# Performance work log

Measured on AMD Instinct MI355X. Metric: run time of the kernel, lower is better.

## Reference

```python
import jax, jax.numpy as jnp
import numpy as np

VOCAB, E, H, L, N = 32000, 256, 512, 512, 64


def setup_inputs() -> dict:
    key = jax.random.key(0)
    ks = jax.random.split(key, 8)
    s_in = 1.0 / np.sqrt(H + E)
    return {
        "x": jax.random.randint(ks[0], (L, N), 0, VOCAB),
        "emb": jax.random.normal(ks[1], (VOCAB, E), dtype=jnp.float32),
        # weights stored (in, out); math identical to torch Linear with W.T
        "Wz": jax.random.uniform(ks[2], (H + E, H), jnp.float32, -s_in, s_in),
        "bz": jax.random.uniform(ks[3], (H,), jnp.float32, -s_in, s_in),
        "Wr": jax.random.uniform(ks[4], (H + E, H), jnp.float32, -s_in, s_in),
        "br": jax.random.uniform(ks[5], (H,), jnp.float32, -s_in, s_in),
        "Wh": jax.random.uniform(ks[6], (H + E, H), jnp.float32, -s_in, s_in),
        "bh": jax.random.uniform(ks[7], (H,), jnp.float32, -s_in, s_in),
    }


def reference(x, emb, Wz, bz, Wr, br, Wh, bh):
    # x: (L, N) int indices -> embedded once: (L, N, E)
    xe = emb[x]
    h0 = jnp.zeros((x.shape[1], Wz.shape[1]), dtype=emb.dtype)

    def step(h, e_t):
        hx = jnp.concatenate([h, e_t], axis=1)            # (N, H+E)
        z = jax.nn.sigmoid(hx @ Wz + bz)                  # update gate
        r = jax.nn.sigmoid(hx @ Wr + br)                  # reset gate
        rhx = jnp.concatenate([r * h, e_t], axis=1)
        h_tilde = jnp.tanh(rhx @ Wh + bh)
        h_new = (1.0 - z) * h + z * h_tilde
        return h_new, h_new

    _, hs = jax.lax.scan(step, h0, xe)                    # hs: (L, N, H)
    return hs
```

## Files before the change

### kernel.cpp

```cpp
#include <hip/hip_runtime.h>


#define LSTEPS 512
#define NBATCH 64
#define HDIM   512
#define EDIM   256
#define KDIM   768
#define NBLK   32
#define TPB    256

typedef _Float16 f16x8 __attribute__((ext_vector_type(8)));
typedef float    f32x4 __attribute__((ext_vector_type(4)));
typedef unsigned long long u64;

#define MFMA __builtin_amdgcn_mfma_f32_16x16x32_f16

__device__ __forceinline__ float sigm(float x){ return 1.0f/(1.0f+__expf(-x)); }
__device__ __forceinline__ float tanh_fast(float x){
  float e = __expf(2.0f*x);
  return 1.0f - 2.0f/(e + 1.0f);
}
__device__ __forceinline__ unsigned f16b(float x){
  union { _Float16 h; unsigned short u; } c; c.h = (_Float16)x; return (unsigned)c.u;
}

__global__ void prep_w(const float* __restrict__ Wz, const float* __restrict__ Wr,
                       const float* __restrict__ Wh, _Float16* __restrict__ wbuf){
  int tid = blockIdx.x*256 + threadIdx.x;
  int g   = tid / (HDIM*KDIM);
  int rem = tid - g*(HDIM*KDIM);
  int j   = rem / KDIM;
  int k   = rem - j*KDIM;
  const float* W = (g==0) ? Wz : ((g==1) ? Wr : Wh);
  wbuf[tid] = (_Float16)W[(size_t)k*HDIM + j];
}

__global__ void prep_emb(const int* __restrict__ x, const float* __restrict__ emb,
                         _Float16* __restrict__ ebuf){
  int tid = blockIdx.x*256 + threadIdx.x;
  int k4  = tid & 63;
  int tn  = tid >> 6;
  int row = x[tn];
  const float4 v = *(const float4*)(emb + (size_t)row*EDIM + (k4<<2));
  union { _Float16 h[4]; uint2 u; } p;
  p.h[0] = (_Float16)v.x; p.h[1] = (_Float16)v.y;
  p.h[2] = (_Float16)v.z; p.h[3] = (_Float16)v.w;
  *(uint2*)(ebuf + (size_t)tn*EDIM + (k4<<2)) = p.u;
}

__device__ __forceinline__ void store_x(_Float16* buf, int jc2, int n0, int lane,
                                        float v0, float v1, float v2, float v3){
  unsigned p01 = f16b(v0) | (f16b(v1) << 16);
  unsigned p23 = f16b(v2) | (f16b(v3) << 16);
  unsigned q01 = __shfl_xor(p01, 1, 64);
  unsigned q23 = __shfl_xor(p23, 1, 64);
  unsigned w0, w1; int r0;
  if (lane & 1){
    w0 = (q23 & 0xffffu) | (p23 << 16);
    w1 = (q23 >> 16)     | (p23 & 0xffff0000u);
    r0 = n0 + 2;
  } else {
    w0 = (p01 & 0xffffu) | (q01 << 16);
    w1 = (p01 >> 16)     | (q01 & 0xffff0000u);
    r0 = n0;
  }
  __hip_atomic_store((unsigned*)(buf + (size_t)r0*HDIM + jc2),     w0,
                     __ATOMIC_RELAXED, __HIP_MEMORY_SCOPE_AGENT);
  __hip_atomic_store((unsigned*)(buf + (size_t)(r0+1)*HDIM + jc2), w1,
                     __ATOMIC_RELAXED, __HIP_MEMORY_SCOPE_AGENT);
}

__device__ __forceinline__ void waitcnt_ge(const unsigned* c, unsigned target){
  for (;;){
    unsigned v = __hip_atomic_load(c, __ATOMIC_RELAXED, __HIP_MEMORY_SCOPE_AGENT);
    if (v >= target) break;
  }
}

__global__ __launch_bounds__(TPB, 1) void gru_persist(
    const _Float16* __restrict__ wbuf,
    const _Float16* __restrict__ ebuf,
    const float* __restrict__ bz, const float* __restrict__ br, const float* __restrict__ bh,
    _Float16* __restrict__ hx,
    _Float16* __restrict__ rhx,
    unsigned* __restrict__ cnth,
    unsigned* __restrict__ cntrh,
    float* __restrict__ out)
{
  __shared__ char wlds[3*16*1536];
  const int jbase = blockIdx.x * 16;

  for (int cidx = threadIdx.x; cidx < 3*16*96; cidx += TPB){
    int g   = cidx / (16*96);
    int rem = cidx - g*(16*96);
    int col = rem / 96;
    int kch = rem - col*96;
    const uint4 v = *(const uint4*)(wbuf + ((size_t)(g*HDIM + jbase + col))*KDIM + kch*8);
    int off = (((g*16 + col)*1536) + kch*16) ^ ((col & 7) << 4);
    *(uint4*)(wlds + off) = v;
  }
  __syncthreads();

  const int lane = threadIdx.x & 63;
  const int wave = threadIdx.x >> 6;
  const int c15  = lane & 15;
  const int kgrp = lane >> 4;
  const int jcol = jbase + c15;
  const int jc2  = jcol & ~1;
  const int arow = wave*16 + c15;
  const int n0   = wave*16 + kgrp*4;
  const int swz  = (c15 & 7) << 4;
  const int linz = ((      c15)*1536) + kgrp*16;
  const int linr = ((16  + c15)*1536) + kgrp*16;
  const int linh = ((32  + c15)*1536) + kgrp*16;
  const float bzj = bz[jcol];
  const float brj = br[jcol];
  const float bhj = bh[jcol];
  unsigned* mycnth  = cnth  + wave*32;
  unsigned* mycntrh = cntrh + wave*32;
  const u64* hrow  = (const u64*)hx  + (size_t)arow*128 + kgrp*2;
  const u64* rhrow = (const u64*)rhx + (size_t)arow*128 + kgrp*2;
  float hreg[4] = {0.f, 0.f, 0.f, 0.f};

  u64 q[32];
  f16x8 aereg[8];

#define LOADX(BASE) do {                                                      \
    _Pragma("unroll")                                                         \
    for (int kc = 0; kc < 16; ++kc){                                          \
      q[2*kc]   = __hip_atomic_load((BASE) + kc*8,     __ATOMIC_RELAXED,      \
                                    __HIP_MEMORY_SCOPE_AGENT);                \
      q[2*kc+1] = __hip_atomic_load((BASE) + kc*8 + 1, __ATOMIC_RELAXED,      \
                                    __HIP_MEMORY_SCOPE_AGENT);                \
    }                                                                         \
  } while (0)

#define AFRAG(KC) ({ union { u64 d[2]; f16x8 v; } _a;                         \
                     _a.d[0] = q[2*(KC)]; _a.d[1] = q[2*(KC)+1]; _a.v; })

  {
    const _Float16* ae0 = ebuf + (size_t)arow*EDIM + kgrp*8;
    #pragma unroll
    for (int kc = 0; kc < 8; ++kc) aereg[kc] = *(const f16x8*)(ae0 + kc*32);
  }

  for (int t = 0; t < LSTEPS; ++t){
    const unsigned tgt_h  = 32u*(unsigned)t;
    const unsigned tgt_rh = 32u*(unsigned)(t + 1);

    f32x4 accr = {0.f,0.f,0.f,0.f};
    #pragma unroll
    for (int kc = 0; kc < 8; ++kc){
      f16x8 brv = *(const f16x8*)(wlds + ((linr + (16+kc)*64) ^ swz));
      accr = MFMA(aereg[kc], brv, accr, 0, 0, 0);
    }
    waitcnt_ge(mycnth, tgt_h);
    LOADX(hrow);
    #pragma unroll
    for (int kc = 0; kc < 16; ++kc){
      f16x8 brv = *(const f16x8*)(wlds + ((linr + kc*64) ^ swz));
      accr = MFMA(AFRAG(kc), brv, accr, 0, 0, 0);
    }
    float rh[4];
    #pragma unroll
    for (int i = 0; i < 4; ++i)
      rh[i] = sigm(accr[i] + brj) * hreg[i];
    store_x(rhx, jc2, n0, lane, rh[0], rh[1], rh[2], rh[3]);
    asm volatile("s_waitcnt vmcnt(0)" ::: "memory");
    __builtin_amdgcn_sched_barrier(0);
    if (lane == 0)
      __hip_atomic_fetch_add(mycntrh, 1u,
                             __ATOMIC_RELAXED, __HIP_MEMORY_SCOPE_AGENT);

    f32x4 accz = {0.f,0.f,0.f,0.f};
    f32x4 acch = {0.f,0.f,0.f,0.f};
    #pragma unroll
    for (int kc = 0; kc < 16; ++kc){
      f16x8 bzv = *(const f16x8*)(wlds + ((linz + kc*64) ^ swz));
      accz = MFMA(AFRAG(kc), bzv, accz, 0, 0, 0);
    }
    #pragma unroll
    for (int kc = 0; kc < 8; ++kc){
      f16x8 bzv = *(const f16x8*)(wlds + ((linz + (16+kc)*64) ^ swz));
      f16x8 bhv = *(const f16x8*)(wlds + ((linh + (16+kc)*64) ^ swz));
      accz = MFMA(aereg[kc], bzv, accz, 0, 0, 0);
      acch = MFMA(aereg[kc], bhv, acch, 0, 0, 0);
    }
    float zreg[4];
    #pragma unroll
    for (int i = 0; i < 4; ++i) zreg[i] = sigm(accz[i] + bzj);

    waitcnt_ge(mycntrh, tgt_rh);
    LOADX(rhrow);
    #pragma unroll
    for (int kc = 0; kc < 16; ++kc){
      f16x8 bhv = *(const f16x8*)(wlds + ((linh + kc*64) ^ swz));
      acch = MFMA(AFRAG(kc), bhv, acch, 0, 0, 0);
    }
    #pragma unroll
    for (int i = 0; i < 4; ++i){
      float ht = tanh_fast(acch[i] + bhj);
      hreg[i] = hreg[i] + zreg[i]*(ht - hreg[i]);
    }
    store_x(hx, jc2, n0, lane, hreg[0], hreg[1], hreg[2], hreg[3]);
    asm volatile("s_waitcnt vmcnt(0)" ::: "memory");
    __builtin_amdgcn_sched_barrier(0);
    if (lane == 0)
      __hip_atomic_fetch_add(mycnth, 1u,
                             __ATOMIC_RELAXED, __HIP_MEMORY_SCOPE_AGENT);

    if (t + 1 < LSTEPS){
      const _Float16* aen = ebuf + ((size_t)(t+1)*NBATCH + arow)*EDIM + kgrp*8;
      #pragma unroll
      for (int kc = 0; kc < 8; ++kc) aereg[kc] = *(const f16x8*)(aen + kc*32);
    }
    #pragma unroll
    for (int i = 0; i < 4; ++i)
      out[((size_t)t*NBATCH + (n0+i))*HDIM + jcol] = hreg[i];
  }
#undef LOADX
#undef AFRAG
}

extern "C" void kernel_launch(void* const* d_in, const int* in_sizes, int n_in,
                              void* d_out, int out_size, void* d_ws, size_t ws_size,
                              hipStream_t stream) {
  const int*   x   = (const int*)  d_in[0];
  const float* emb = (const float*)d_in[1];
  const float* Wz  = (const float*)d_in[2];
  const float* bz  = (const float*)d_in[3];
  const float* Wr  = (const float*)d_in[4];
  const float* br  = (const float*)d_in[5];
  const float* Wh  = (const float*)d_in[6];
  const float* bh  = (const float*)d_in[7];
  float* out = (float*)d_out;
  char*  ws  = (char*)d_ws;

  size_t off = 0;
  unsigned* cnth  = (unsigned*)(ws + off); off += 4*32*4;
  unsigned* cntrh = (unsigned*)(ws + off); off += 4*32*4;
  _Float16* hx    = (_Float16*)(ws + off); off += (size_t)NBATCH*HDIM*2;
  size_t zero_bytes = off;
  _Float16* rhx   = (_Float16*)(ws + off); off += (size_t)NBATCH*HDIM*2;
  _Float16* wbuf  = (_Float16*)(ws + off); off += (size_t)3*HDIM*KDIM*2;
  _Float16* ebuf  = (_Float16*)(ws + off); off += (size_t)LSTEPS*NBATCH*EDIM*2;

  hipMemsetAsync(ws, 0, zero_bytes, stream);

  prep_w  <<<(3*HDIM*KDIM)/256,          256, 0, stream>>>(Wz, Wr, Wh, wbuf);
  prep_emb<<<(LSTEPS*NBATCH*EDIM/4)/256, 256, 0, stream>>>(x, emb, ebuf);
  gru_persist<<<NBLK, TPB, 0, stream>>>(wbuf, ebuf, bz, br, bh,
                                        hx, rhx, cnth, cntrh, out);
}
```

Measured before the change: 6.253 ms.

## Replace atomic step counters with per-block flags polled across lanes

Instead of every block doing a fetch_add on a shared per-wave counter, each block now stores the step index into its own flag slot. Waiters load all 32 block flags in parallel across lanes and leave the spin loop when every flag has reached the target. The out stores and the next-step embedding prefetch are moved off the critical path between releases, and the release now waits with a partial vmcnt so outstanding prefetch loads do not hold it up. The change also adds a startup probe that tests cross-XCD coherence of a flag/data pair and runs a burn loop if that test fails; this adds risk and possible overhead.

Result: no change. 6.302 ms (+0.8%).

```diff
diff --git a/kernel.cpp b/kernel.cpp
--- a/kernel.cpp
+++ b/kernel.cpp
@@ -70,10 +70,11 @@
                      __ATOMIC_RELAXED, __HIP_MEMORY_SCOPE_AGENT);
 }
 
-__device__ __forceinline__ void waitcnt_ge(const unsigned* c, unsigned target){
+__device__ __forceinline__ void waitfl(const unsigned* fl, unsigned target){
+  const int l31 = threadIdx.x & 31;
   for (;;){
-    unsigned v = __hip_atomic_load(c, __ATOMIC_RELAXED, __HIP_MEMORY_SCOPE_AGENT);
-    if (v >= target) break;
+    unsigned v = __hip_atomic_load(&fl[l31], __ATOMIC_RELAXED, __HIP_MEMORY_SCOPE_AGENT);
+    if (__all(v >= target)) break;
   }
 }
 
@@ -83,11 +84,15 @@
     const float* __restrict__ bz, const float* __restrict__ br, const float* __restrict__ bh,
     _Float16* __restrict__ hx,
     _Float16* __restrict__ rhx,
-    unsigned* __restrict__ cnth,
-    unsigned* __restrict__ cntrh,
+    unsigned* __restrict__ hfl,
+    unsigned* __restrict__ rhfl,
+    unsigned* __restrict__ xcnt,
+    unsigned* __restrict__ cflag,
+    unsigned* __restrict__ cdata,
     float* __restrict__ out)
 {
   __shared__ char wlds[3*16*1536];
+  __shared__ int s_role, s_burn;
   const int jbase = blockIdx.x * 16;
 
   for (int cidx = threadIdx.x; cidx < 3*16*96; cidx += TPB){
@@ -100,6 +105,56 @@
     *(uint4*)(wlds + off) = v;
   }
   __syncthreads();
+
+  if (threadIdx.x == 0){
+    unsigned xcd;
+    asm volatile("s_getreg_b32 %0, hwreg(HW_REG_XCC_ID)" : "=s"(xcd));
+    xcd &= 7;
+    unsigned rank = __hip_atomic_fetch_add(&xcnt[xcd], 1u,
+                        __ATOMIC_RELAXED, __HIP_MEMORY_SCOPE_AGENT);
+    s_role = (rank == 0) ? (int)(xcd<<1) : ((rank == 1) ? (int)((xcd<<1)|1) : -1);
+    s_burn = 0;
+  }
+  __syncthreads();
+  {
+    const int role = s_role;
+    if (role >= 0 && (role & 1) == 0){
+      if (threadIdx.x == 0){
+        int xcd = role >> 1;
+        *(volatile unsigned*)&cdata[xcd*16] = 0xC0FFEE00u + (unsigned)xcd;
+        asm volatile("s_waitcnt vmcnt(0)" ::: "memory");
+        __hip_atomic_store(&cflag[xcd*16], 1u, __ATOMIC_RELAXED, __HIP_MEMORY_SCOPE_AGENT);
+      }
+    }
+    if (role >= 0 && (role & 1) == 1){
+      if (threadIdx.x == 0){
+        int xcd = role >> 1;
+        volatile unsigned* dp = &cdata[xcd*16];
+        unsigned pre = *dp; (void)pre;
+        int ok = 0;
+        for (int i = 0; i < (1<<15); ++i){
+          if (__hip_atomic_load(&cflag[xcd*16], __ATOMIC_RELAXED,
+                                __HIP_MEMORY_SCOPE_AGENT) == 1u){ ok = 1; break; }
+        }
+        unsigned v = 0;
+        if (ok){
+          asm volatile("buffer_inv" ::: "memory");
+          asm volatile("s_waitcnt vmcnt(0)" ::: "memory");
+          v = *dp;
+        }
+        s_burn = (ok && v == 0xC0FFEE00u + (unsigned)xcd) ? 0 : 1;
+      }
+      __syncthreads();
+      if (s_burn && (threadIdx.x >> 6) == 0){
+        const float* src = out + (size_t)(role >> 1) * 2097152;
+        float acc = 0.f;
+        for (int i = (threadIdx.x & 63); i < 2097152; i += 256)
+          acc += src[i];
+        asm volatile("" :: "v"(acc));
+      }
+      __syncthreads();
+    }
+  }
 
   const int lane = threadIdx.x & 63;
   const int wave = threadIdx.x >> 6;
@@ -116,8 +171,8 @@
   const float bzj = bz[jcol];
   const float brj = br[jcol];
   const float bhj = bh[jcol];
-  unsigned* mycnth  = cnth  + wave*32;
-  unsigned* mycntrh = cntrh + wave*32;
+  unsigned* myhfl  = hfl  + wave*32;
+  unsigned* myrhfl = rhfl + wave*32;
   const u64* hrow  = (const u64*)hx  + (size_t)arow*128 + kgrp*2;
   const u64* rhrow = (const u64*)rhx + (size_t)arow*128 + kgrp*2;
   float hreg[4] = {0.f, 0.f, 0.f, 0.f};
@@ -145,16 +200,24 @@
   }
 
   for (int t = 0; t < LSTEPS; ++t){
-    const unsigned tgt_h  = 32u*(unsigned)t;
-    const unsigned tgt_rh = 32u*(unsigned)(t + 1);
-
     f32x4 accr = {0.f,0.f,0.f,0.f};
     #pragma unroll
     for (int kc = 0; kc < 8; ++kc){
       f16x8 brv = *(const f16x8*)(wlds + ((linr + (16+kc)*64) ^ swz));
       accr = MFMA(aereg[kc], brv, accr, 0, 0, 0);
     }
-    waitcnt_ge(mycnth, tgt_h);
+    asm volatile("s_waitcnt vmcnt(0)" ::: "memory");
+    __builtin_amdgcn_sched_barrier(0);
+    if (lane == 0)
+      __hip_atomic_store(&myhfl[blockIdx.x], (unsigned)t,
+                         __ATOMIC_RELAXED, __HIP_MEMORY_SCOPE_AGENT);
+    if (t > 0){
+      #pragma unroll
+      for (int i = 0; i < 4; ++i)
+        out[((size_t)(t-1)*NBATCH + (n0+i))*HDIM + jcol] = hreg[i];
+    }
+
+    waitfl(myhfl, (unsigned)t);
     LOADX(hrow);
     #pragma unroll
     for (int kc = 0; kc < 16; ++kc){
@@ -166,11 +229,7 @@
     for (int i = 0; i < 4; ++i)
       rh[i] = sigm(accr[i] + brj) * hreg[i];
     store_x(rhx, jc2, n0, lane, rh[0], rh[1], rh[2], rh[3]);
-    asm volatile("s_waitcnt vmcnt(0)" ::: "memory");
-    __builtin_amdgcn_sched_barrier(0);
-    if (lane == 0)
-      __hip_atomic_fetch_add(mycntrh, 1u,
-                             __ATOMIC_RELAXED, __HIP_MEMORY_SCOPE_AGENT);
+    asm volatile("" ::: "memory");
 
     f32x4 accz = {0.f,0.f,0.f,0.f};
     f32x4 acch = {0.f,0.f,0.f,0.f};
@@ -186,11 +245,24 @@
       accz = MFMA(aereg[kc], bzv, accz, 0, 0, 0);
       acch = MFMA(aereg[kc], bhv, acch, 0, 0, 0);
     }
+    {
+      const int tn = (t + 1 < LSTEPS) ? (t + 1) : t;
+      const _Float16* aen = ebuf + ((size_t)tn*NBATCH + arow)*EDIM + kgrp*8;
+      #pragma unroll
+      for (int kc = 0; kc < 8; ++kc) aereg[kc] = *(const f16x8*)(aen + kc*32);
+    }
+    asm volatile("" ::: "memory");
+    __builtin_amdgcn_sched_barrier(0);
+    asm volatile("s_waitcnt vmcnt(8)" ::: "memory");
+    __builtin_amdgcn_sched_barrier(0);
+    if (lane == 0)
+      __hip_atomic_store(&myrhfl[blockIdx.x], (unsigned)(t + 1),
+                         __ATOMIC_RELAXED, __HIP_MEMORY_SCOPE_AGENT);
     float zreg[4];
     #pragma unroll
     for (int i = 0; i < 4; ++i) zreg[i] = sigm(accz[i] + bzj);
 
-    waitcnt_ge(mycntrh, tgt_rh);
+    waitfl(myrhfl, (unsigned)(t + 1));
     LOADX(rhrow);
     #pragma unroll
     for (int kc = 0; kc < 16; ++kc){
@@ -203,21 +275,11 @@
       hreg[i] = hreg[i] + zreg[i]*(ht - hreg[i]);
     }
     store_x(hx, jc2, n0, lane, hreg[0], hreg[1], hreg[2], hreg[3]);
-    asm volatile("s_waitcnt vmcnt(0)" ::: "memory");
-    __builtin_amdgcn_sched_barrier(0);
-    if (lane == 0)
-      __hip_atomic_fetch_add(mycnth, 1u,
-                             __ATOMIC_RELAXED, __HIP_MEMORY_SCOPE_AGENT);
-
-    if (t + 1 < LSTEPS){
-      const _Float16* aen = ebuf + ((size_t)(t+1)*NBATCH + arow)*EDIM + kgrp*8;
-      #pragma unroll
-      for (int kc = 0; kc < 8; ++kc) aereg[kc] = *(const f16x8*)(aen + kc*32);
-    }
-    #pragma unroll
-    for (int i = 0; i < 4; ++i)
-      out[((size_t)t*NBATCH + (n0+i))*HDIM + jcol] = hreg[i];
-  }
+  }
+  asm volatile("s_waitcnt vmcnt(0)" ::: "memory");
+  #pragma unroll
+  for (int i = 0; i < 4; ++i)
+    out[((size_t)(LSTEPS-1)*NBATCH + (n0+i))*HDIM + jcol] = hreg[i];
 #undef LOADX
 #undef AFRAG
 }
@@ -237,8 +299,11 @@
   char*  ws  = (char*)d_ws;
 
   size_t off = 0;
-  unsigned* cnth  = (unsigned*)(ws + off); off += 4*32*4;
-  unsigned* cntrh = (unsigned*)(ws + off); off += 4*32*4;
+  unsigned* hfl   = (unsigned*)(ws + off); off += 4*32*4;
+  unsigned* rhfl  = (unsigned*)(ws + off); off += 4*32*4;
+  unsigned* xcnt  = (unsigned*)(ws + off); off += 64;
+  unsigned* cflag = (unsigned*)(ws + off); off += 8*16*4;
+  unsigned* cdata = (unsigned*)(ws + off); off += 8*16*4;
   _Float16* hx    = (_Float16*)(ws + off); off += (size_t)NBATCH*HDIM*2;
   size_t zero_bytes = off;
   _Float16* rhx   = (_Float16*)(ws + off); off += (size_t)NBATCH*HDIM*2;
@@ -250,5 +315,6 @@
   prep_w  <<<(3*HDIM*KDIM)/256,          256, 0, stream>>>(Wz, Wr, Wh, wbuf);
   prep_emb<<<(LSTEPS*NBATCH*EDIM/4)/256, 256, 0, stream>>>(x, emb, ebuf);
   gru_persist<<<NBLK, TPB, 0, stream>>>(wbuf, ebuf, bz, br, bh,
-                                        hx, rhx, cnth, cntrh, out);
-}
+                                        hx, rhx, hfl, rhfl,
+                                        xcnt, cflag, cdata, out);
+}
```

## Co-locate GRU workers on one XCD and sync through local L2 flags

Applied to the files above, without the earlier changes.

Launches 128 blocks and elects the first XCD to gather 16 blocks; those 16 become the only workers, each owning 32 hidden columns instead of 16. The goal is to keep all cross-block exchange of h and r*h inside one XCD's L2, avoiding device-scope MALL round trips. The old shared counters become per-block tag flags that are polled with a warp vote. Each write goes to both an L2 copy and a MALL copy, and waiting falls back to the MALL path after a spin budget, trading extra stores and idle launched blocks for lower step latency.

Measured after the change: 5.921 ms. -5.3%, faster.

```diff
diff --git a/kernel.cpp b/kernel.cpp
--- a/kernel.cpp
+++ b/kernel.cpp
@@ -6,8 +6,11 @@
 #define HDIM   512
 #define EDIM   256
 #define KDIM   768
-#define NBLK   32
+#define NWORK  16
+#define COLS   32
 #define TPB    256
+#define NLAUNCH 128
+#define FASTBUDGET 300
 
 typedef _Float16 f16x8 __attribute__((ext_vector_type(8)));
 typedef float    f32x4 __attribute__((ext_vector_type(4)));
@@ -22,6 +25,16 @@
 }
 __device__ __forceinline__ unsigned f16b(float x){
   union { _Float16 h; unsigned short u; } c; c.h = (_Float16)x; return (unsigned)c.u;
+}
+__device__ __forceinline__ f16x8 AFU(u64 a, u64 b){
+  union { u64 d[2]; f16x8 v; } c; c.d[0] = a; c.d[1] = b; return c.v;
+}
+
+__device__ __forceinline__ unsigned ld_sc0_u32(const unsigned* a){
+  unsigned r;
+  asm volatile("global_load_dword %0, %1, off sc0\n\ts_waitcnt vmcnt(0)"
+               : "=v"(r) : "v"(a) : "memory");
+  return r;
 }
 
 __global__ void prep_w(const float* __restrict__ Wz, const float* __restrict__ Wr,
@@ -48,55 +61,101 @@
   *(uint2*)(ebuf + (size_t)tn*EDIM + (k4<<2)) = p.u;
 }
 
-__device__ __forceinline__ void store_x(_Float16* buf, int jc2, int n0, int lane,
-                                        float v0, float v1, float v2, float v3){
+__device__ __forceinline__ void pack2(int lane, float v0, float v1, float v2,
+                                      float v3, unsigned* w0, unsigned* w1, int* r0){
   unsigned p01 = f16b(v0) | (f16b(v1) << 16);
   unsigned p23 = f16b(v2) | (f16b(v3) << 16);
   unsigned q01 = __shfl_xor(p01, 1, 64);
   unsigned q23 = __shfl_xor(p23, 1, 64);
-  unsigned w0, w1; int r0;
   if (lane & 1){
-    w0 = (q23 & 0xffffu) | (p23 << 16);
-    w1 = (q23 >> 16)     | (p23 & 0xffff0000u);
-    r0 = n0 + 2;
+    *w0 = (q23 & 0xffffu) | (p23 << 16);
+    *w1 = (q23 >> 16)     | (p23 & 0xffff0000u);
+    *r0 = 2;
   } else {
-    w0 = (p01 & 0xffffu) | (q01 << 16);
-    w1 = (p01 >> 16)     | (q01 & 0xffff0000u);
-    r0 = n0;
-  }
-  __hip_atomic_store((unsigned*)(buf + (size_t)r0*HDIM + jc2),     w0,
+    *w0 = (p01 & 0xffffu) | (q01 << 16);
+    *w1 = (p01 >> 16)     | (q01 & 0xffff0000u);
+    *r0 = 0;
+  }
+}
+
+__device__ __forceinline__ void store_dual(_Float16* bufL2, _Float16* bufM,
+                                           int jc2, int n0, int lane,
+                                           float v0, float v1, float v2, float v3){
+  unsigned w0, w1; int rr;
+  pack2(lane, v0, v1, v2, v3, &w0, &w1, &rr);
+  int r0 = n0 + rr;
+  *(unsigned*)(bufL2 + (size_t)r0*HDIM + jc2)     = w0;
+  *(unsigned*)(bufL2 + (size_t)(r0+1)*HDIM + jc2) = w1;
+  __hip_atomic_store((unsigned*)(bufM + (size_t)r0*HDIM + jc2),     w0,
                      __ATOMIC_RELAXED, __HIP_MEMORY_SCOPE_AGENT);
-  __hip_atomic_store((unsigned*)(buf + (size_t)(r0+1)*HDIM + jc2), w1,
+  __hip_atomic_store((unsigned*)(bufM + (size_t)(r0+1)*HDIM + jc2), w1,
                      __ATOMIC_RELAXED, __HIP_MEMORY_SCOPE_AGENT);
 }
 
-__device__ __forceinline__ void waitcnt_ge(const unsigned* c, unsigned target){
+__device__ __forceinline__ int waitx(const unsigned* flL2, const unsigned* flM,
+                                     unsigned target, int fpd){
+  const int l15 = threadIdx.x & 15;
+  if (!fpd){
+    for (int i = 0; i < FASTBUDGET; ++i){
+      unsigned v = ld_sc0_u32(flL2 + l15);
+      if (__all((int)(v >= target))) return 0;
+    }
+  }
   for (;;){
-    unsigned v = __hip_atomic_load(c, __ATOMIC_RELAXED, __HIP_MEMORY_SCOPE_AGENT);
-    if (v >= target) break;
-  }
+    unsigned v = __hip_atomic_load(flM + l15, __ATOMIC_RELAXED,
+                                   __HIP_MEMORY_SCOPE_AGENT);
+    if (__all((int)(v >= target))) break;
+  }
+  return 1;
 }
 
 __global__ __launch_bounds__(TPB, 1) void gru_persist(
     const _Float16* __restrict__ wbuf,
     const _Float16* __restrict__ ebuf,
     const float* __restrict__ bz, const float* __restrict__ br, const float* __restrict__ bh,
-    _Float16* __restrict__ hx,
-    _Float16* __restrict__ rhx,
-    unsigned* __restrict__ cnth,
-    unsigned* __restrict__ cntrh,
+    _Float16* __restrict__ hxL, _Float16* __restrict__ hxM,
+    _Float16* __restrict__ rhL, _Float16* __restrict__ rhM,
+    unsigned* __restrict__ hflL, unsigned* __restrict__ hflM,
+    unsigned* __restrict__ rflL, unsigned* __restrict__ rflM,
+    unsigned* __restrict__ xcnt, unsigned* __restrict__ winner,
     float* __restrict__ out)
 {
-  __shared__ char wlds[3*16*1536];
-  const int jbase = blockIdx.x * 16;
-
-  for (int cidx = threadIdx.x; cidx < 3*16*96; cidx += TPB){
-    int g   = cidx / (16*96);
-    int rem = cidx - g*(16*96);
+  __shared__ char wlds[3*COLS*1536];
+  __shared__ int s_slot;
+
+  if (threadIdx.x == 0){
+    unsigned xcd;
+    asm volatile("s_getreg_b32 %0, hwreg(HW_REG_XCC_ID)" : "=s"(xcd));
+    xcd &= 7;
+    unsigned rank = __hip_atomic_fetch_add(&xcnt[xcd], 1u,
+                        __ATOMIC_RELAXED, __HIP_MEMORY_SCOPE_AGENT);
+    int slot = -1;
+    if (rank < NWORK){
+      if (rank == NWORK-1){
+        unsigned exp = 0u;
+        __hip_atomic_compare_exchange_strong(winner, &exp, xcd+1u,
+            __ATOMIC_RELAXED, __ATOMIC_RELAXED, __HIP_MEMORY_SCOPE_AGENT);
+      }
+      unsigned w;
+      do { w = __hip_atomic_load(winner, __ATOMIC_RELAXED,
+                                 __HIP_MEMORY_SCOPE_AGENT); }
+      while (w == 0u);
+      if (w == xcd+1u) slot = (int)rank;
+    }
+    s_slot = slot;
+  }
+  __syncthreads();
+  const int slot = s_slot;
+  if (slot < 0) return;
+
+  const int jbase = slot * COLS;
+  for (int cidx = threadIdx.x; cidx < 3*COLS*96; cidx += TPB){
+    int g   = cidx / (COLS*96);
+    int rem = cidx - g*(COLS*96);
     int col = rem / 96;
     int kch = rem - col*96;
     const uint4 v = *(const uint4*)(wbuf + ((size_t)(g*HDIM + jbase + col))*KDIM + kch*8);
-    int off = (((g*16 + col)*1536) + kch*16) ^ ((col & 7) << 4);
+    int off = (((g*COLS + col)*1536) + kch*16) ^ ((col & 7) << 4);
     *(uint4*)(wlds + off) = v;
   }
   __syncthreads();
@@ -105,27 +164,46 @@
   const int wave = threadIdx.x >> 6;
   const int c15  = lane & 15;
   const int kgrp = lane >> 4;
-  const int jcol = jbase + c15;
-  const int jc2  = jcol & ~1;
   const int arow = wave*16 + c15;
   const int n0   = wave*16 + kgrp*4;
   const int swz  = (c15 & 7) << 4;
-  const int linz = ((      c15)*1536) + kgrp*16;
-  const int linr = ((16  + c15)*1536) + kgrp*16;
-  const int linh = ((32  + c15)*1536) + kgrp*16;
-  const float bzj = bz[jcol];
-  const float brj = br[jcol];
-  const float bhj = bh[jcol];
-  unsigned* mycnth  = cnth  + wave*32;
-  unsigned* mycntrh = cntrh + wave*32;
-  const u64* hrow  = (const u64*)hx  + (size_t)arow*128 + kgrp*2;
-  const u64* rhrow = (const u64*)rhx + (size_t)arow*128 + kgrp*2;
-  float hreg[4] = {0.f, 0.f, 0.f, 0.f};
+  const int jcol0 = jbase + c15;
+  const int jcol1 = jbase + 16 + c15;
+  const int jc20  = jcol0 & ~1;
+  const int jc21  = jcol1 & ~1;
+  const int lz0 = ((0*COLS + c15     )*1536) + kgrp*16;
+  const int lz1 = ((0*COLS + c15 + 16)*1536) + kgrp*16;
+  const int lr0 = ((1*COLS + c15     )*1536) + kgrp*16;
+  const int lr1 = ((1*COLS + c15 + 16)*1536) + kgrp*16;
+  const int lh0 = ((2*COLS + c15     )*1536) + kgrp*16;
+  const int lh1 = ((2*COLS + c15 + 16)*1536) + kgrp*16;
+  const float bzj0 = bz[jcol0], bzj1 = bz[jcol1];
+  const float brj0 = br[jcol0], brj1 = br[jcol1];
+  const float bhj0 = bh[jcol0], bhj1 = bh[jcol1];
+  const u64* hrowL = (const u64*)hxL + (size_t)arow*128 + kgrp*2;
+  const u64* hrowM = (const u64*)hxM + (size_t)arow*128 + kgrp*2;
+  const u64* rrowL = (const u64*)rhL + (size_t)arow*128 + kgrp*2;
+  const u64* rrowM = (const u64*)rhM + (size_t)arow*128 + kgrp*2;
+  unsigned* myhflL = hflL + wave*NWORK;
+  unsigned* myhflM = hflM + wave*NWORK;
+  unsigned* myrflL = rflL + wave*NWORK;
+  unsigned* myrflM = rflM + wave*NWORK;
+  float hreg0[4] = {0,0,0,0}, hreg1[4] = {0,0,0,0};
+  int fpd = 0;
 
   u64 q[32];
   f16x8 aereg[8];
 
-#define LOADX(BASE) do {                                                      \
+#define LOADQ_FAST(BASE) do {                                                 \
+    asm volatile("buffer_inv" ::: "memory");                                  \
+    _Pragma("unroll")                                                         \
+    for (int kc = 0; kc < 16; ++kc){                                          \
+      q[2*kc]   = (BASE)[kc*8];                                               \
+      q[2*kc+1] = (BASE)[kc*8 + 1];                                           \
+    }                                                                         \
+  } while (0)
+
+#define LOADQ_MALL(BASE) do {                                                 \
     _Pragma("unroll")                                                         \
     for (int kc = 0; kc < 16; ++kc){                                          \
       q[2*kc]   = __hip_atomic_load((BASE) + kc*8,     __ATOMIC_RELAXED,      \
@@ -135,9 +213,6 @@
     }                                                                         \
   } while (0)
 
-#define AFRAG(KC) ({ union { u64 d[2]; f16x8 v; } _a;                         \
-                     _a.d[0] = q[2*(KC)]; _a.d[1] = q[2*(KC)+1]; _a.v; })
-
   {
     const _Float16* ae0 = ebuf + (size_t)arow*EDIM + kgrp*8;
     #pragma unroll
@@ -145,81 +220,117 @@
   }
 
   for (int t = 0; t < LSTEPS; ++t){
-    const unsigned tgt_h  = 32u*(unsigned)t;
-    const unsigned tgt_rh = 32u*(unsigned)(t + 1);
-
-    f32x4 accr = {0.f,0.f,0.f,0.f};
+    const unsigned tagn = (unsigned)(t + 1);
+
+    f32x4 accr0 = {0,0,0,0}, accr1 = {0,0,0,0};
     #pragma unroll
     for (int kc = 0; kc < 8; ++kc){
-      f16x8 brv = *(const f16x8*)(wlds + ((linr + (16+kc)*64) ^ swz));
-      accr = MFMA(aereg[kc], brv, accr, 0, 0, 0);
-    }
-    waitcnt_ge(mycnth, tgt_h);
-    LOADX(hrow);
+      f16x8 b0 = *(const f16x8*)(wlds + ((lr0 + (16+kc)*64) ^ swz));
+      f16x8 b1 = *(const f16x8*)(wlds + ((lr1 + (16+kc)*64) ^ swz));
+      accr0 = MFMA(aereg[kc], b0, accr0, 0, 0, 0);
+      accr1 = MFMA(aereg[kc], b1, accr1, 0, 0, 0);
+    }
+    {
+      int fb = waitx(myhflL, myhflM, (unsigned)t, fpd);
+      fpd |= fb;
+      if (fb) LOADQ_MALL(hrowM); else LOADQ_FAST(hrowL);
+    }
     #pragma unroll
     for (int kc = 0; kc < 16; ++kc){
-      f16x8 brv = *(const f16x8*)(wlds + ((linr + kc*64) ^ swz));
-      accr = MFMA(AFRAG(kc), brv, accr, 0, 0, 0);
-    }
-    float rh[4];
-    #pragma unroll
-    for (int i = 0; i < 4; ++i)
-      rh[i] = sigm(accr[i] + brj) * hreg[i];
-    store_x(rhx, jc2, n0, lane, rh[0], rh[1], rh[2], rh[3]);
+      f16x8 a  = AFU(q[2*kc], q[2*kc+1]);
+      f16x8 b0 = *(const f16x8*)(wlds + ((lr0 + kc*64) ^ swz));
+      f16x8 b1 = *(const f16x8*)(wlds + ((lr1 + kc*64) ^ swz));
+      accr0 = MFMA(a, b0, accr0, 0, 0, 0);
+      accr1 = MFMA(a, b1, accr1, 0, 0, 0);
+    }
+    float rh0[4], rh1[4];
+    #pragma unroll
+    for (int i = 0; i < 4; ++i){
+      rh0[i] = sigm(accr0[i] + brj0) * hreg0[i];
+      rh1[i] = sigm(accr1[i] + brj1) * hreg1[i];
+    }
+    store_dual(rhL, rhM, jc20, n0, lane, rh0[0], rh0[1], rh0[2], rh0[3]);
+    store_dual(rhL, rhM, jc21, n0, lane, rh1[0], rh1[1], rh1[2], rh1[3]);
     asm volatile("s_waitcnt vmcnt(0)" ::: "memory");
     __builtin_amdgcn_sched_barrier(0);
-    if (lane == 0)
-      __hip_atomic_fetch_add(mycntrh, 1u,
-                             __ATOMIC_RELAXED, __HIP_MEMORY_SCOPE_AGENT);
-
-    f32x4 accz = {0.f,0.f,0.f,0.f};
-    f32x4 acch = {0.f,0.f,0.f,0.f};
+    if (lane == 0){
+      *(volatile unsigned*)&myrflL[slot] = tagn;
+      __hip_atomic_store(&myrflM[slot], tagn,
+                         __ATOMIC_RELAXED, __HIP_MEMORY_SCOPE_AGENT);
+    }
+
+    f32x4 accz0 = {0,0,0,0}, accz1 = {0,0,0,0};
+    f32x4 acch0 = {0,0,0,0}, acch1 = {0,0,0,0};
     #pragma unroll
     for (int kc = 0; kc < 16; ++kc){
-      f16x8 bzv = *(const f16x8*)(wlds + ((linz + kc*64) ^ swz));
-      accz = MFMA(AFRAG(kc), bzv, accz, 0, 0, 0);
+      f16x8 a  = AFU(q[2*kc], q[2*kc+1]);
+      f16x8 b0 = *(const f16x8*)(wlds + ((lz0 + kc*64) ^ swz));
+      f16x8 b1 = *(const f16x8*)(wlds + ((lz1 + kc*64) ^ swz));
+      accz0 = MFMA(a, b0, accz0, 0, 0, 0);
+      accz1 = MFMA(a, b1, accz1, 0, 0, 0);
     }
     #pragma unroll
     for (int kc = 0; kc < 8; ++kc){
-      f16x8 bzv = *(const f16x8*)(wlds + ((linz + (16+kc)*64) ^ swz));
-      f16x8 bhv = *(const f16x8*)(wlds + ((linh + (16+kc)*64) ^ swz));
-      accz = MFMA(aereg[kc], bzv, accz, 0, 0, 0);
-      acch = MFMA(aereg[kc], bhv, acch, 0, 0, 0);
-    }
-    float zreg[4];
-    #pragma unroll
-    for (int i = 0; i < 4; ++i) zreg[i] = sigm(accz[i] + bzj);
-
-    waitcnt_ge(mycntrh, tgt_rh);
-    LOADX(rhrow);
+      f16x8 z0 = *(const f16x8*)(wlds + ((lz0 + (16+kc)*64) ^ swz));
+      f16x8 z1 = *(const f16x8*)(wlds + ((lz1 + (16+kc)*64) ^ swz));
+      f16x8 h0 = *(const f16x8*)(wlds + ((lh0 + (16+kc)*64) ^ swz));
+      f16x8 h1 = *(const f16x8*)(wlds + ((lh1 + (16+kc)*64) ^ swz));
+      accz0 = MFMA(aereg[kc], z0, accz0, 0, 0, 0);
+      accz1 = MFMA(aereg[kc], z1, accz1, 0, 0, 0);
+      acch0 = MFMA(aereg[kc], h0, acch0, 0, 0, 0);
+      acch1 = MFMA(aereg[kc], h1, acch1, 0, 0, 0);
+    }
+    float zreg0[4], zreg1[4];
+    #pragma unroll
+    for (int i = 0; i < 4; ++i){
+      zreg0[i] = sigm(accz0[i] + bzj0);
+      zreg1[i] = sigm(accz1[i] + bzj1);
+    }
+
+    {
+      int fb = waitx(myrflL, myrflM, tagn, fpd);
+      fpd |= fb;
+      if (fb) LOADQ_MALL(rrowM); else LOADQ_FAST(rrowL);
+    }
     #pragma unroll
     for (int kc = 0; kc < 16; ++kc){
-      f16x8 bhv = *(const f16x8*)(wlds + ((linh + kc*64) ^ swz));
-      acch = MFMA(AFRAG(kc), bhv, acch, 0, 0, 0);
+      f16x8 a  = AFU(q[2*kc], q[2*kc+1]);
+      f16x8 b0 = *(const f16x8*)(wlds + ((lh0 + kc*64) ^ swz));
+      f16x8 b1 = *(const f16x8*)(wlds + ((lh1 + kc*64) ^ swz));
+      acch0 = MFMA(a, b0, acch0, 0, 0, 0);
+      acch1 = MFMA(a, b1, acch1, 0, 0, 0);
     }
     #pragma unroll
     for (int i = 0; i < 4; ++i){
-      float ht = tanh_fast(acch[i] + bhj);
-      hreg[i] = hreg[i] + zreg[i]*(ht - hreg[i]);
-    }
-    store_x(hx, jc2, n0, lane, hreg[0], hreg[1], hreg[2], hreg[3]);
+      float ht0 = tanh_fast(acch0[i] + bhj0);
+      float ht1 = tanh_fast(acch1[i] + bhj1);
+      hreg0[i] = hreg0[i] + zreg0[i]*(ht0 - hreg0[i]);
+      hreg1[i] = hreg1[i] + zreg1[i]*(ht1 - hreg1[i]);
+    }
+    store_dual(hxL, hxM, jc20, n0, lane, hreg0[0], hreg0[1], hreg0[2], hreg0[3]);
+    store_dual(hxL, hxM, jc21, n0, lane, hreg1[0], hreg1[1], hreg1[2], hreg1[3]);
     asm volatile("s_waitcnt vmcnt(0)" ::: "memory");
     __builtin_amdgcn_sched_barrier(0);
-    if (lane == 0)
-      __hip_atomic_fetch_add(mycnth, 1u,
-                             __ATOMIC_RELAXED, __HIP_MEMORY_SCOPE_AGENT);
-
+    if (lane == 0){
+      *(volatile unsigned*)&myhflL[slot] = tagn;
+      __hip_atomic_store(&myhflM[slot], tagn,
+                         __ATOMIC_RELAXED, __HIP_MEMORY_SCOPE_AGENT);
+    }
+
+    #pragma unroll
+    for (int i = 0; i < 4; ++i){
+      int n = n0 + i;
+      out[((size_t)t*NBATCH + n)*HDIM + jcol0] = hreg0[i];
+      out[((size_t)t*NBATCH + n)*HDIM + jcol1] = hreg1[i];
+    }
     if (t + 1 < LSTEPS){
       const _Float16* aen = ebuf + ((size_t)(t+1)*NBATCH + arow)*EDIM + kgrp*8;
       #pragma unroll
       for (int kc = 0; kc < 8; ++kc) aereg[kc] = *(const f16x8*)(aen + kc*32);
     }
-    #pragma unroll
-    for (int i = 0; i < 4; ++i)
-      out[((size_t)t*NBATCH + (n0+i))*HDIM + jcol] = hreg[i];
-  }
-#undef LOADX
-#undef AFRAG
+  }
+#undef LOADQ_FAST
+#undef LOADQ_MALL
 }
 
 extern "C" void kernel_launch(void* const* d_in, const int* in_sizes, int n_in,
@@ -237,18 +348,26 @@
   char*  ws  = (char*)d_ws;
 
   size_t off = 0;
-  unsigned* cnth  = (unsigned*)(ws + off); off += 4*32*4;
-  unsigned* cntrh = (unsigned*)(ws + off); off += 4*32*4;
-  _Float16* hx    = (_Float16*)(ws + off); off += (size_t)NBATCH*HDIM*2;
+  unsigned* xcnt   = (unsigned*)(ws + off); off += 64;
+  unsigned* winner = (unsigned*)(ws + off); off += 64;
+  unsigned* hflL = (unsigned*)(ws + off); off += 4*NWORK*4;
+  unsigned* hflM = (unsigned*)(ws + off); off += 4*NWORK*4;
+  unsigned* rflL = (unsigned*)(ws + off); off += 4*NWORK*4;
+  unsigned* rflM = (unsigned*)(ws + off); off += 4*NWORK*4;
+  _Float16* hxL  = (_Float16*)(ws + off); off += (size_t)NBATCH*HDIM*2;
+  _Float16* hxM  = (_Float16*)(ws + off); off += (size_t)NBATCH*HDIM*2;
   size_t zero_bytes = off;
-  _Float16* rhx   = (_Float16*)(ws + off); off += (size_t)NBATCH*HDIM*2;
-  _Float16* wbuf  = (_Float16*)(ws + off); off += (size_t)3*HDIM*KDIM*2;
-  _Float16* ebuf  = (_Float16*)(ws + off); off += (size_t)LSTEPS*NBATCH*EDIM*2;
+  _Float16* rhL  = (_Float16*)(ws + off); off += (size_t)NBATCH*HDIM*2;
+  _Float16* rhM  = (_Float16*)(ws + off); off += (size_t)NBATCH*HDIM*2;
+  _Float16* wbuf = (_Float16*)(ws + off); off += (size_t)3*HDIM*KDIM*2;
+  _Float16* ebuf = (_Float16*)(ws + off); off += (size_t)LSTEPS*NBATCH*EDIM*2;
 
   hipMemsetAsync(ws, 0, zero_bytes, stream);
 
   prep_w  <<<(3*HDIM*KDIM)/256,          256, 0, stream>>>(Wz, Wr, Wh, wbuf);
   prep_emb<<<(LSTEPS*NBATCH*EDIM/4)/256, 256, 0, stream>>>(x, emb, ebuf);
-  gru_persist<<<NBLK, TPB, 0, stream>>>(wbuf, ebuf, bz, br, bh,
-                                        hx, rhx, cnth, cntrh, out);
-}
+  gru_persist<<<NLAUNCH, TPB, 0, stream>>>(wbuf, ebuf, bz, br, bh,
+                                           hxL, hxM, rhL, rhM,
+                                           hflL, hflM, rflL, rflM,
+                                           xcnt, winner, out);
+}
```
